# Kernel tuning notes

Measured on AMD Instinct MI355X. Metric: run time of the kernel, lower is better.

## Reference

```python
import jax, jax.numpy as jnp
import numpy as np

# Fixed-step Dormand-Prince RK45 (dopri5) over t in [0, 1].
# torchdiffeq's dopri5 is adaptive; an adaptive while-loop is not
# reverse-differentiable in JAX, so we use the same dopri5 tableau with a
# fixed step count, which reproduces the per-step math exactly.
N_STEPS = 64

# dopri5 Butcher tableau (a-matrix rows; b = 5th-order weights = row a7)
A21 = 1/5
A31, A32 = 3/40, 9/40
A41, A42, A43 = 44/45, -56/15, 32/9
A51, A52, A53, A54 = 19372/6561, -25360/2187, 64448/6561, -212/729
A61, A62, A63, A64, A65 = 9017/3168, -355/33, 46732/5247, 49/176, -5103/18656
B1, B3, B4, B5, B6 = 35/384, 500/1113, 125/192, -2187/6784, 11/84


def setup_inputs() -> dict:
    key = jax.random.key(0)
    ks = jax.random.split(key, 7)
    data_dim, hidden_dim, batch = 512, 1024, 4096
    s1 = 1.0 / np.sqrt(data_dim)
    s2 = 1.0 / np.sqrt(hidden_dim)
    return {
        "x":  jax.random.normal(ks[0], (batch, data_dim), jnp.float32),
        "W1": jax.random.normal(ks[1], (hidden_dim, data_dim), jnp.float32) * s1,
        "b1": jax.random.normal(ks[2], (hidden_dim,), jnp.float32) * s1,
        "W2": jax.random.normal(ks[3], (hidden_dim, hidden_dim), jnp.float32) * s2,
        "b2": jax.random.normal(ks[4], (hidden_dim,), jnp.float32) * s2,
        "W3": jax.random.normal(ks[5], (data_dim, hidden_dim), jnp.float32) * s2,
        "b3": jax.random.normal(ks[6], (data_dim,), jnp.float32) * s2,
    }


def reference(x, W1, b1, W2, b2, W3, b3):
    def f(y):  # ODEFunc MLP: fc1 -> relu -> fc2 -> relu -> fc3 (autonomous)
        h = jax.nn.relu(y @ W1.T + b1)
        h = jax.nn.relu(h @ W2.T + b2)
        return h @ W3.T + b3

    h = jnp.float32(1.0 / N_STEPS)

    def step(y, _):
        k1 = f(y)
        k2 = f(y + h * (A21 * k1))
        k3 = f(y + h * (A31 * k1 + A32 * k2))
        k4 = f(y + h * (A41 * k1 + A42 * k2 + A43 * k3))
        k5 = f(y + h * (A51 * k1 + A52 * k2 + A53 * k3 + A54 * k4))
        k6 = f(y + h * (A61 * k1 + A62 * k2 + A63 * k3 + A64 * k4 + A65 * k5))
        y_next = y + h * (B1 * k1 + B3 * k3 + B4 * k4 + B5 * k5 + B6 * k6)
        return y_next, None

    y_final, _ = jax.lax.scan(step, x, None, length=N_STEPS)
    return y_final
```

## Files before the change

### kernel.cpp

```cpp
#include <hip/hip_runtime.h>
#include <hip/hip_bf16.h>
#include <stdint.h>
#include <stddef.h>

using bf16_t = __hip_bfloat16;
typedef __attribute__((ext_vector_type(8))) short short8;
typedef __attribute__((ext_vector_type(4))) float f32x4;

__device__ __forceinline__ void gload_lds16(void* lds, const void* g) {
  __builtin_amdgcn_global_load_lds(
      (const __attribute__((address_space(1))) unsigned int*)g,
      (__attribute__((address_space(3))) unsigned int*)lds,
      16, 0, 0);
}

template<int MODE>
__global__ __launch_bounds__(256, 4)
void gemm_bt(const bf16_t* __restrict__ A, const bf16_t* __restrict__ B,
             const float* __restrict__ bias,
             bf16_t* __restrict__ obf,
             bf16_t* __restrict__ kout,
             float* __restrict__ yf_out,
             const float* __restrict__ y_in,
             const bf16_t* __restrict__ kp0, const bf16_t* __restrict__ kp1,
             const bf16_t* __restrict__ kp2, const bf16_t* __restrict__ kp3,
             float c0, float c1, float c2, float c3, float ccur,
             int M, int N, int K, int lgx)
{
  __shared__ __align__(16) bf16_t As[2][64 * 64];
  __shared__ __align__(16) bf16_t Bs[2][64 * 64];

  const int t    = threadIdx.x;
  const int lane = t & 63;
  const int wid  = t >> 6;
  const int wm   = wid >> 1;
  const int wn   = wid & 1;

  const int nwg = gridDim.x, bid = blockIdx.x;
  const int swz = (bid & 7) * (nwg >> 3) + (bid >> 3);
  const int gxm = (1 << lgx) - 1;
  const int bx  = swz & gxm;
  const int by  = swz >> lgx;
  const int bn0 = bx * 64, bm0 = by * 64;

  const bf16_t* Ag = A + (size_t)bm0 * K;
  const bf16_t* Bg = B + (size_t)bn0 * K;

  f32x4 acc[2][2] = {};

  auto stage = [&](int b, int kt) {
    const int k0 = kt * 64;
#pragma unroll
    for (int r = 0; r < 2; ++r) {
      int ch  = t + r * 256;
      int row = ch >> 3, s = ch & 7;
      int sl  = s ^ (row & 7);
      gload_lds16(&As[b][ch * 8], Ag + (size_t)row * K + k0 + sl * 8);
    }
#pragma unroll
    for (int r = 0; r < 2; ++r) {
      int ch  = t + r * 256;
      int row = ch >> 3, s = ch & 7;
      int sl  = s ^ (row & 7);
      gload_lds16(&Bs[b][ch * 8], Bg + (size_t)row * K + k0 + sl * 8);
    }
  };

  const int nt = K >> 6;
  stage(0, 0);

  const int ro = lane & 15;
  const int ks = lane >> 4;

  for (int tt = 0; tt < nt; ++tt) {
    const int c = tt & 1;
    asm volatile("s_waitcnt vmcnt(0)" ::: "memory");
    __builtin_amdgcn_s_barrier();
    asm volatile("" ::: "memory");

    if (tt + 1 < nt) stage(c ^ 1, tt + 1);

#pragma unroll
    for (int kk = 0; kk < 2; ++kk) {
      short8 af[2], bfr[2];
      const int slot = kk * 4 + ks;
#pragma unroll
      for (int mi = 0; mi < 2; ++mi) {
        int row = wm * 32 + mi * 16 + ro;
        int ch  = row * 8 + (slot ^ (row & 7));
        af[mi]  = *(const short8*)&As[c][ch * 8];
      }
#pragma unroll
      for (int ni = 0; ni < 2; ++ni) {
        int row = wn * 32 + ni * 16 + ro;
        int ch  = row * 8 + (slot ^ (row & 7));
        bfr[ni] = *(const short8*)&Bs[c][ch * 8];
      }
      __builtin_amdgcn_s_setprio(1);
#pragma unroll
      for (int mi = 0; mi < 2; ++mi)
#pragma unroll
        for (int ni = 0; ni < 2; ++ni)
          acc[mi][ni] = __builtin_amdgcn_mfma_f32_16x16x32_bf16(
              af[mi], bfr[ni], acc[mi][ni], 0, 0, 0);
      __builtin_amdgcn_s_setprio(0);
    }
  }

  const int rb = bm0 + wm * 32;
  const int cb = bn0 + wn * 32;
#pragma unroll
  for (int mi = 0; mi < 2; ++mi) {
#pragma unroll
    for (int ni = 0; ni < 2; ++ni) {
      const int col = cb + ni * 16 + ro;
      const float bv = bias[col];
#pragma unroll
      for (int r = 0; r < 4; ++r) {
        const int row = rb + mi * 16 + (lane >> 4) * 4 + r;
        const size_t idx = (size_t)row * N + col;
        float v = acc[mi][ni][r] + bv;
        if (MODE == 0) {
          obf[idx] = __float2bfloat16(fmaxf(v, 0.f));
        } else {
          if (MODE == 1) kout[idx] = __float2bfloat16(v);
          float z = y_in[idx] + ccur * v;
          if (kp0) z += c0 * __bfloat162float(kp0[idx]);
          if (kp1) z += c1 * __bfloat162float(kp1[idx]);
          if (kp2) z += c2 * __bfloat162float(kp2[idx]);
          if (kp3) z += c3 * __bfloat162float(kp3[idx]);
          if (MODE == 2) yf_out[idx] = z;
          obf[idx] = __float2bfloat16(z);
        }
      }
    }
  }
}

__global__ void init_all(const float* __restrict__ x,
                         const float* __restrict__ W1,
                         const float* __restrict__ W2,
                         const float* __restrict__ W3,
                         bf16_t* __restrict__ W1b, bf16_t* __restrict__ W2b,
                         bf16_t* __restrict__ W3b,
                         float* __restrict__ y, bf16_t* __restrict__ yb,
                         int n1, int n2, int n3, int ny)
{
  const int gt = blockIdx.x * blockDim.x + threadIdx.x;
  const int gs = gridDim.x * blockDim.x;
  auto cvt4 = [&](const float* in, bf16_t* outp, int n) {
    for (int i = gt * 4; i < n; i += gs * 4) {
      float4 v = *(const float4*)(in + i);
      bf16_t o[4] = {__float2bfloat16(v.x), __float2bfloat16(v.y),
                     __float2bfloat16(v.z), __float2bfloat16(v.w)};
      *(uint64_t*)(outp + i) = *(uint64_t*)o;
    }
  };
  cvt4(W1, W1b, n1);
  cvt4(W2, W2b, n2);
  cvt4(W3, W3b, n3);
  for (int i = gt * 4; i < ny; i += gs * 4) {
    float4 v = *(const float4*)(x + i);
    *(float4*)(y + i) = v;
    bf16_t o[4] = {__float2bfloat16(v.x), __float2bfloat16(v.y),
                   __float2bfloat16(v.z), __float2bfloat16(v.w)};
    *(uint64_t*)(yb + i) = *(uint64_t*)o;
  }
}

extern "C" void kernel_launch(void* const* d_in, const int* in_sizes, int n_in,
                              void* d_out, int out_size, void* d_ws, size_t ws_size,
                              hipStream_t stream)
{
  const float* x  = (const float*)d_in[0];
  const float* W1 = (const float*)d_in[1];
  const float* b1 = (const float*)d_in[2];
  const float* W2 = (const float*)d_in[3];
  const float* b2 = (const float*)d_in[4];
  const float* W3 = (const float*)d_in[5];
  const float* b3 = (const float*)d_in[6];

  const int data   = in_sizes[6];
  const int hidden = in_sizes[2];
  const int batch  = in_sizes[0] / data;

  char* ws = (char*)d_ws;
  size_t off = 0;
  auto alloc = [&](size_t bytes) -> void* {
    off = (off + 255) & ~(size_t)255;
    void* p = ws + off;
    off += bytes;
    return p;
  };
  const size_t nyd = (size_t)batch * data;
  const size_t nh  = (size_t)batch * hidden;

  float*  y   = (float*)alloc(nyd * 4);
  bf16_t* yb  = (bf16_t*)alloc(nyd * 2);
  bf16_t* zb  = (bf16_t*)alloc(nyd * 2);
  bf16_t* h1  = (bf16_t*)alloc(nh * 2);
  bf16_t* h2  = (bf16_t*)alloc(nh * 2);
  bf16_t* k1  = (bf16_t*)alloc(nyd * 2);
  bf16_t* k2  = (bf16_t*)alloc(nyd * 2);
  bf16_t* k3  = (bf16_t*)alloc(nyd * 2);
  bf16_t* k4  = (bf16_t*)alloc(nyd * 2);
  bf16_t* k5  = (bf16_t*)alloc(nyd * 2);
  bf16_t* W1b = (bf16_t*)alloc((size_t)hidden * data * 2);
  bf16_t* W2b = (bf16_t*)alloc((size_t)hidden * hidden * 2);
  bf16_t* W3b = (bf16_t*)alloc((size_t)data * hidden * 2);

  init_all<<<2048, 256, 0, stream>>>(x, W1, W2, W3, W1b, W2b, W3b, y, yb,
                                     hidden * data, hidden * hidden,
                                     data * hidden, (int)nyd);

  const double hh = 1.0 / 64.0;
  const float hA21 = (float)(hh * (1.0/5.0));
  const float hA31 = (float)(hh * (3.0/40.0)),    hA32 = (float)(hh * (9.0/40.0));
  const float hA41 = (float)(hh * (44.0/45.0)),   hA42 = (float)(hh * (-56.0/15.0)),
              hA43 = (float)(hh * (32.0/9.0));
  const float hA51 = (float)(hh * (19372.0/6561.0)),  hA52 = (float)(hh * (-25360.0/2187.0)),
              hA53 = (float)(hh * (64448.0/6561.0)),  hA54 = (float)(hh * (-212.0/729.0));
  const float hA61 = (float)(hh * (9017.0/3168.0)),   hA62 = (float)(hh * (-355.0/33.0)),
              hA63 = (float)(hh * (46732.0/5247.0)),  hA64 = (float)(hh * (49.0/176.0)),
              hA65 = (float)(hh * (-5103.0/18656.0));
  const float hB1 = (float)(hh * (35.0/384.0)),   hB3 = (float)(hh * (500.0/1113.0)),
              hB4 = (float)(hh * (125.0/192.0)),  hB5 = (float)(hh * (-2187.0/6784.0)),
              hB6 = (float)(hh * (11.0/84.0));

  const dim3 blk(256);
  const int gridH = (hidden / 64) * (batch / 64);
  const int grid3 = (data / 64) * (batch / 64);
  const int lgxH = 4, lgx3 = 3;

  auto mlp_front = [&](const bf16_t* zin) {
    gemm_bt<0><<<gridH, blk, 0, stream>>>(
        zin, W1b, b1, h1, nullptr, nullptr, nullptr,
        nullptr, nullptr, nullptr, nullptr, 0.f, 0.f, 0.f, 0.f, 0.f,
        batch, hidden, data, lgxH);
    gemm_bt<0><<<gridH, blk, 0, stream>>>(
        h1, W2b, b2, h2, nullptr, nullptr, nullptr,
        nullptr, nullptr, nullptr, nullptr, 0.f, 0.f, 0.f, 0.f, 0.f,
        batch, hidden, hidden, lgxH);
  };

  auto stage_k = [&](bf16_t* kout, const bf16_t* p0, float cc0, const bf16_t* p1, float cc1,
                     const bf16_t* p2, float cc2, const bf16_t* p3, float cc3, float ccur) {
    gemm_bt<1><<<grid3, blk, 0, stream>>>(
        h2, W3b, b3, zb, kout, nullptr, y,
        p0, p1, p2, p3, cc0, cc1, cc2, cc3, ccur,
        batch, data, hidden, lgx3);
  };

  for (int step = 0; step < 64; ++step) {
    mlp_front(yb);
    stage_k(k1, nullptr, 0.f, nullptr, 0.f, nullptr, 0.f, nullptr, 0.f, hA21);
    mlp_front(zb);
    stage_k(k2, k1, hA31, nullptr, 0.f, nullptr, 0.f, nullptr, 0.f, hA32);
    mlp_front(zb);
    stage_k(k3, k1, hA41, k2, hA42, nullptr, 0.f, nullptr, 0.f, hA43);
    mlp_front(zb);
    stage_k(k4, k1, hA51, k2, hA52, k3, hA53, nullptr, 0.f, hA54);
    mlp_front(zb);
    stage_k(k5, k1, hA61, k2, hA62, k3, hA63, k4, hA64, hA65);
    mlp_front(zb);
    float* yf = (step == 63) ? (float*)d_out : y;
    gemm_bt<2><<<grid3, blk, 0, stream>>>(
        h2, W3b, b3, yb, nullptr, yf, y,
        k1, k3, k4, k5, hB1, hB3, hB4, hB5, hB6,
        batch, data, hidden, lgx3);
  }
}
```

Before: 18.22 ms.

## Load B fragments directly to registers and enlarge M tile for hidden GEMMs

The GEMM kernel becomes a templated core. It stages only A through LDS and loads the B (weight) MFMA fragments straight from global memory into registers, double-buffered. The hidden-layer GEMMs use a 128-row M tile (MFRAG=4) with launch bounds lowered to 2 waves per SIMD, which halves their grid and improves A reuse. This removes B LDS traffic and barriers, at the cost of uncoalesced direct global loads of B, more register pressure, and a main loop unrolled by two that assumes an even K-tile count.

```diff
diff --git a/kernel.cpp b/kernel.cpp
--- a/kernel.cpp
+++ b/kernel.cpp
@@ -14,21 +14,21 @@
       16, 0, 0);
 }
 
-template<int MODE>
-__global__ __launch_bounds__(256, 4)
-void gemm_bt(const bf16_t* __restrict__ A, const bf16_t* __restrict__ B,
-             const float* __restrict__ bias,
-             bf16_t* __restrict__ obf,
-             bf16_t* __restrict__ kout,
-             float* __restrict__ yf_out,
-             const float* __restrict__ y_in,
-             const bf16_t* __restrict__ kp0, const bf16_t* __restrict__ kp1,
-             const bf16_t* __restrict__ kp2, const bf16_t* __restrict__ kp3,
-             float c0, float c1, float c2, float c3, float ccur,
-             int M, int N, int K, int lgx)
+template<int MFRAG, int MODE>
+__device__ __forceinline__ void gemm_core(
+    const bf16_t* __restrict__ A, const bf16_t* __restrict__ B,
+    const float* __restrict__ bias,
+    bf16_t* __restrict__ obf,
+    bf16_t* __restrict__ kout,
+    float* __restrict__ yf_out,
+    const float* __restrict__ y_in,
+    const bf16_t* __restrict__ kp0, const bf16_t* __restrict__ kp1,
+    const bf16_t* __restrict__ kp2, const bf16_t* __restrict__ kp3,
+    float c0, float c1, float c2, float c3, float ccur,
+    int M, int N, int K, int lgx)
 {
-  __shared__ __align__(16) bf16_t As[2][64 * 64];
-  __shared__ __align__(16) bf16_t Bs[2][64 * 64];
+  constexpr int BM = 32 * MFRAG;
+  __shared__ __align__(16) bf16_t As[2][BM * 64];
 
   const int t    = threadIdx.x;
   const int lane = t & 63;
@@ -41,76 +41,86 @@
   const int gxm = (1 << lgx) - 1;
   const int bx  = swz & gxm;
   const int by  = swz >> lgx;
-  const int bn0 = bx * 64, bm0 = by * 64;
+  const int bn0 = bx * 64, bm0 = by * BM;
+
+  const int ro = lane & 15;
+  const int ks = lane >> 4;
 
   const bf16_t* Ag = A + (size_t)bm0 * K;
-  const bf16_t* Bg = B + (size_t)bn0 * K;
-
-  f32x4 acc[2][2] = {};
-
-  auto stage = [&](int b, int kt) {
+  const bf16_t* Bcol = B + (size_t)(bn0 + wn * 32 + ro) * K + ks * 8;
+
+  auto stageA = [&](int b, int kt) {
     const int k0 = kt * 64;
 #pragma unroll
-    for (int r = 0; r < 2; ++r) {
+    for (int r = 0; r < MFRAG; ++r) {
       int ch  = t + r * 256;
       int row = ch >> 3, s = ch & 7;
       int sl  = s ^ (row & 7);
       gload_lds16(&As[b][ch * 8], Ag + (size_t)row * K + k0 + sl * 8);
     }
-#pragma unroll
-    for (int r = 0; r < 2; ++r) {
-      int ch  = t + r * 256;
-      int row = ch >> 3, s = ch & 7;
-      int sl  = s ^ (row & 7);
-      gload_lds16(&Bs[b][ch * 8], Bg + (size_t)row * K + k0 + sl * 8);
+  };
+  auto loadB = [&](short8* dst, int kt) {
+#pragma unroll
+    for (int ni = 0; ni < 2; ++ni)
+#pragma unroll
+      for (int kk = 0; kk < 2; ++kk)
+        dst[ni * 2 + kk] =
+            *(const short8*)(Bcol + (size_t)ni * 16 * K + kt * 64 + kk * 32);
+  };
+
+  f32x4 acc[MFRAG][2] = {};
+
+  auto compute = [&](const bf16_t* lds, const short8* bfr) {
+#pragma unroll
+    for (int kk = 0; kk < 2; ++kk) {
+      short8 af[MFRAG];
+      const int slot = kk * 4 + ks;
+#pragma unroll
+      for (int mi = 0; mi < MFRAG; ++mi) {
+        int row = wm * (MFRAG * 16) + mi * 16 + ro;
+        int ch  = row * 8 + (slot ^ (row & 7));
+        af[mi]  = *(const short8*)&lds[ch * 8];
+      }
+      __builtin_amdgcn_s_setprio(1);
+#pragma unroll
+      for (int mi = 0; mi < MFRAG; ++mi)
+#pragma unroll
+        for (int ni = 0; ni < 2; ++ni)
+          acc[mi][ni] = __builtin_amdgcn_mfma_f32_16x16x32_bf16(
+              af[mi], bfr[ni * 2 + kk], acc[mi][ni], 0, 0, 0);
+      __builtin_amdgcn_s_setprio(0);
     }
   };
 
   const int nt = K >> 6;
-  stage(0, 0);
-
-  const int ro = lane & 15;
-  const int ks = lane >> 4;
-
-  for (int tt = 0; tt < nt; ++tt) {
-    const int c = tt & 1;
+  short8 b0[4], b1[4];
+  stageA(0, 0);
+  loadB(b0, 0);
+
+  for (int tt = 0; tt < nt; tt += 2) {
     asm volatile("s_waitcnt vmcnt(0)" ::: "memory");
     __builtin_amdgcn_s_barrier();
     asm volatile("" ::: "memory");
-
-    if (tt + 1 < nt) stage(c ^ 1, tt + 1);
-
-#pragma unroll
-    for (int kk = 0; kk < 2; ++kk) {
-      short8 af[2], bfr[2];
-      const int slot = kk * 4 + ks;
-#pragma unroll
-      for (int mi = 0; mi < 2; ++mi) {
-        int row = wm * 32 + mi * 16 + ro;
-        int ch  = row * 8 + (slot ^ (row & 7));
-        af[mi]  = *(const short8*)&As[c][ch * 8];
-      }
-#pragma unroll
-      for (int ni = 0; ni < 2; ++ni) {
-        int row = wn * 32 + ni * 16 + ro;
-        int ch  = row * 8 + (slot ^ (row & 7));
-        bfr[ni] = *(const short8*)&Bs[c][ch * 8];
-      }
-      __builtin_amdgcn_s_setprio(1);
-#pragma unroll
-      for (int mi = 0; mi < 2; ++mi)
-#pragma unroll
-        for (int ni = 0; ni < 2; ++ni)
-          acc[mi][ni] = __builtin_amdgcn_mfma_f32_16x16x32_bf16(
-              af[mi], bfr[ni], acc[mi][ni], 0, 0, 0);
-      __builtin_amdgcn_s_setprio(0);
-    }
+    {
+      stageA(1, tt + 1);
+      loadB(b1, tt + 1);
+    }
+    compute(As[0], b0);
+
+    asm volatile("s_waitcnt vmcnt(0)" ::: "memory");
+    __builtin_amdgcn_s_barrier();
+    asm volatile("" ::: "memory");
+    if (tt + 2 < nt) {
+      stageA(0, tt + 2);
+      loadB(b0, tt + 2);
+    }
+    compute(As[1], b1);
   }
 
-  const int rb = bm0 + wm * 32;
+  const int rb = bm0 + wm * (MFRAG * 16);
   const int cb = bn0 + wn * 32;
 #pragma unroll
-  for (int mi = 0; mi < 2; ++mi) {
+  for (int mi = 0; mi < MFRAG; ++mi) {
 #pragma unroll
     for (int ni = 0; ni < 2; ++ni) {
       const int col = cb + ni * 16 + ro;
@@ -137,7 +147,25 @@
   }
 }
 
-__global__ void init_all(const float* __restrict__ x,
+#define GEMM_ARGS                                                           \
+    const bf16_t* A, const bf16_t* B, const float* bias, bf16_t* obf,       \
+    bf16_t* kout, float* yf_out, const float* y_in,                         \
+    const bf16_t* kp0, const bf16_t* kp1, const bf16_t* kp2,                \
+    const bf16_t* kp3, float c0, float c1, float c2, float c3, float ccur,  \
+    int M, int N, int K, int lgx
+#define GEMM_PASS A,B,bias,obf,kout,yf_out,y_in,kp0,kp1,kp2,kp3,c0,c1,c2,c3,ccur,M,N,K,lgx
+
+extern "C" __global__ void __launch_bounds__(256, 2) g12relu(GEMM_ARGS) {
+  gemm_core<4, 0>(GEMM_PASS);
+}
+extern "C" __global__ void __launch_bounds__(256, 2) g3kcomb(GEMM_ARGS) {
+  gemm_core<2, 1>(GEMM_PASS);
+}
+extern "C" __global__ void __launch_bounds__(256, 2) g3ycomb(GEMM_ARGS) {
+  gemm_core<2, 2>(GEMM_PASS);
+}
+
+extern "C" __global__ void init_all(const float* __restrict__ x,
                          const float* __restrict__ W1,
                          const float* __restrict__ W2,
                          const float* __restrict__ W3,
@@ -228,16 +256,16 @@
               hB6 = (float)(hh * (11.0/84.0));
 
   const dim3 blk(256);
-  const int gridH = (hidden / 64) * (batch / 64);
+  const int gridH = (hidden / 64) * (batch / 128);
   const int grid3 = (data / 64) * (batch / 64);
   const int lgxH = 4, lgx3 = 3;
 
   auto mlp_front = [&](const bf16_t* zin) {
-    gemm_bt<0><<<gridH, blk, 0, stream>>>(
+    g12relu<<<gridH, blk, 0, stream>>>(
         zin, W1b, b1, h1, nullptr, nullptr, nullptr,
         nullptr, nullptr, nullptr, nullptr, 0.f, 0.f, 0.f, 0.f, 0.f,
         batch, hidden, data, lgxH);
-    gemm_bt<0><<<gridH, blk, 0, stream>>>(
+    g12relu<<<gridH, blk, 0, stream>>>(
         h1, W2b, b2, h2, nullptr, nullptr, nullptr,
         nullptr, nullptr, nullptr, nullptr, 0.f, 0.f, 0.f, 0.f, 0.f,
         batch, hidden, hidden, lgxH);
@@ -245,7 +273,7 @@
 
   auto stage_k = [&](bf16_t* kout, const bf16_t* p0, float cc0, const bf16_t* p1, float cc1,
                      const bf16_t* p2, float cc2, const bf16_t* p3, float cc3, float ccur) {
-    gemm_bt<1><<<grid3, blk, 0, stream>>>(
+    g3kcomb<<<grid3, blk, 0, stream>>>(
         h2, W3b, b3, zb, kout, nullptr, y,
         p0, p1, p2, p3, cc0, cc1, cc2, cc3, ccur,
         batch, data, hidden, lgx3);
@@ -264,7 +292,7 @@
     stage_k(k5, k1, hA61, k2, hA62, k3, hA63, k4, hA64, hA65);
     mlp_front(zb);
     float* yf = (step == 63) ? (float*)d_out : y;
-    gemm_bt<2><<<grid3, blk, 0, stream>>>(
+    g3ycomb<<<grid3, blk, 0, stream>>>(
         h2, W3b, b3, yb, nullptr, yf, y,
         k1, k3, k4, k5, hB1, hB3, hB4, hB5, hB6,
         batch, data, hidden, lgx3);
```

Measured after the change: 24.67 ms. 1.35x slower.

## Fold fc3 into fc1 via precomputed W1·W3 and integrate in hidden space

Applied to the files above, without the earlier changes.

Precomputes W13 = W1·W3 and per-stage folded biases, so each RK stage goes straight from h2 to the next fc1 pre-activation with a 1024x1024 GEMM. Stage pre-activations are kept as bf16 hidden-space vectors. A weighted sum of h2 over the stages is accumulated in the fc2 epilogue, so only one final fc3 GEMM per step updates y. This cuts kernel launches per step and removes the separate fc3-then-fc1 round trip through the 512-wide state. Total FLOPs stay about the same, but the intermediate buffers are twice as wide, and the extra bf16 rounding (W13, stage vectors, the running bf16 sum) adds accuracy risk.

```diff
diff --git a/kernel.cpp b/kernel.cpp
--- a/kernel.cpp
+++ b/kernel.cpp
@@ -15,17 +15,18 @@
 }
 
 template<int MODE>
-__global__ __launch_bounds__(256, 4)
-void gemm_bt(const bf16_t* __restrict__ A, const bf16_t* __restrict__ B,
-             const float* __restrict__ bias,
-             bf16_t* __restrict__ obf,
-             bf16_t* __restrict__ kout,
-             float* __restrict__ yf_out,
-             const float* __restrict__ y_in,
-             const bf16_t* __restrict__ kp0, const bf16_t* __restrict__ kp1,
-             const bf16_t* __restrict__ kp2, const bf16_t* __restrict__ kp3,
-             float c0, float c1, float c2, float c3, float ccur,
-             int M, int N, int K, int lgx)
+__device__ __forceinline__ void gemm_core(
+    const bf16_t* __restrict__ A, const bf16_t* __restrict__ B,
+    const float* __restrict__ bias,
+    bf16_t* __restrict__ obf,
+    bf16_t* __restrict__ aux,
+    bf16_t* __restrict__ vout,
+    float* __restrict__ yf_out,
+    const float* __restrict__ y_in,
+    const bf16_t* __restrict__ p0, const bf16_t* __restrict__ p1,
+    const bf16_t* __restrict__ p2, const bf16_t* __restrict__ p3,
+    float c0, float c1, float c2, float c3, float ccur, int hinit,
+    int M, int N, int K, int lgx)
 {
   __shared__ __align__(16) bf16_t As[2][64 * 64];
   __shared__ __align__(16) bf16_t Bs[2][64 * 64];
@@ -77,7 +78,6 @@
     asm volatile("s_waitcnt vmcnt(0)" ::: "memory");
     __builtin_amdgcn_s_barrier();
     asm volatile("" ::: "memory");
-
     if (tt + 1 < nt) stage(c ^ 1, tt + 1);
 
 #pragma unroll
@@ -114,22 +114,35 @@
 #pragma unroll
     for (int ni = 0; ni < 2; ++ni) {
       const int col = cb + ni * 16 + ro;
-      const float bv = bias[col];
+      const float bv = bias ? bias[col] : 0.f;
 #pragma unroll
       for (int r = 0; r < 4; ++r) {
         const int row = rb + mi * 16 + (lane >> 4) * 4 + r;
         const size_t idx = (size_t)row * N + col;
-        float v = acc[mi][ni][r] + bv;
+        const float a = acc[mi][ni][r];
         if (MODE == 0) {
-          obf[idx] = __float2bfloat16(fmaxf(v, 0.f));
+          float v = fmaxf(a + bv, 0.f);
+          obf[idx] = __float2bfloat16(v);
+          if (aux) {
+            float hs = ccur * v + (hinit ? 0.f : __bfloat162float(aux[idx]));
+            aux[idx] = __float2bfloat16(hs);
+          }
+        } else if (MODE == 1) {
+          vout[idx] = __float2bfloat16(a);
+          float u = __bfloat162float(aux[idx]) + ccur * a + bv;
+          if (p0) u += c0 * __bfloat162float(p0[idx]);
+          if (p1) u += c1 * __bfloat162float(p1[idx]);
+          if (p2) u += c2 * __bfloat162float(p2[idx]);
+          if (p3) u += c3 * __bfloat162float(p3[idx]);
+          obf[idx] = __float2bfloat16(fmaxf(u, 0.f));
+        } else if (MODE == 2) {
+          aux[idx] = __float2bfloat16(a);
+          obf[idx] = __float2bfloat16(fmaxf(a + bv, 0.f));
+        } else if (MODE == 3) {
+          obf[idx] = __float2bfloat16(a);
         } else {
-          if (MODE == 1) kout[idx] = __float2bfloat16(v);
-          float z = y_in[idx] + ccur * v;
-          if (kp0) z += c0 * __bfloat162float(kp0[idx]);
-          if (kp1) z += c1 * __bfloat162float(kp1[idx]);
-          if (kp2) z += c2 * __bfloat162float(kp2[idx]);
-          if (kp3) z += c3 * __bfloat162float(kp3[idx]);
-          if (MODE == 2) yf_out[idx] = z;
+          float z = y_in[idx] + a + ccur * bv;
+          yf_out[idx] = z;
           obf[idx] = __float2bfloat16(z);
         }
       }
@@ -137,14 +150,31 @@
   }
 }
 
-__global__ void init_all(const float* __restrict__ x,
-                         const float* __restrict__ W1,
-                         const float* __restrict__ W2,
-                         const float* __restrict__ W3,
-                         bf16_t* __restrict__ W1b, bf16_t* __restrict__ W2b,
-                         bf16_t* __restrict__ W3b,
-                         float* __restrict__ y, bf16_t* __restrict__ yb,
-                         int n1, int n2, int n3, int ny)
+#define GARGS                                                               \
+    const bf16_t* A, const bf16_t* B, const float* bias, bf16_t* obf,       \
+    bf16_t* aux, bf16_t* vout, float* yf_out, const float* y_in,            \
+    const bf16_t* p0, const bf16_t* p1, const bf16_t* p2, const bf16_t* p3, \
+    float c0, float c1, float c2, float c3, float ccur, int hinit,          \
+    int M, int N, int K, int lgx
+#define GPASS A,B,bias,obf,aux,vout,yf_out,y_in,p0,p1,p2,p3,c0,c1,c2,c3,ccur,hinit,M,N,K,lgx
+
+extern "C" __global__ void __launch_bounds__(256, 4) gmid(GARGS) { gemm_core<0>(GPASS); }
+extern "C" __global__ void __launch_bounds__(256, 4) gvst(GARGS) { gemm_core<1>(GPASS); }
+extern "C" __global__ void __launch_bounds__(256, 4) gyw1(GARGS) { gemm_core<2>(GPASS); }
+extern "C" __global__ void __launch_bounds__(256, 4) gw13(GARGS) { gemm_core<3>(GPASS); }
+extern "C" __global__ void __launch_bounds__(256, 4) gyup(GARGS) { gemm_core<4>(GPASS); }
+
+extern "C" __global__ void init_all(
+    const float* __restrict__ x,
+    const float* __restrict__ W1, const float* __restrict__ W2,
+    const float* __restrict__ W3,
+    const float* __restrict__ b1, const float* __restrict__ b3,
+    bf16_t* __restrict__ W1b, bf16_t* __restrict__ W2b,
+    bf16_t* __restrict__ W3b, bf16_t* __restrict__ W3Tb,
+    float* __restrict__ y, bf16_t* __restrict__ yb,
+    float* __restrict__ bS2, float* __restrict__ bS3, float* __restrict__ bS4,
+    float* __restrict__ bS5, float* __restrict__ bS6,
+    float s2, float s3, float s4, float s5, float s6)
 {
   const int gt = blockIdx.x * blockDim.x + threadIdx.x;
   const int gs = gridDim.x * blockDim.x;
@@ -156,15 +186,30 @@
       *(uint64_t*)(outp + i) = *(uint64_t*)o;
     }
   };
-  cvt4(W1, W1b, n1);
-  cvt4(W2, W2b, n2);
-  cvt4(W3, W3b, n3);
-  for (int i = gt * 4; i < ny; i += gs * 4) {
+  cvt4(W1, W1b, 1024 * 512);
+  cvt4(W2, W2b, 1024 * 1024);
+  cvt4(W3, W3b, 512 * 1024);
+  for (int i = gt; i < 512 * 1024; i += gs) {
+    int d = i >> 10, j = i & 1023;
+    W3Tb[(size_t)j * 512 + d] = __float2bfloat16(W3[i]);
+  }
+  for (int i = gt * 4; i < 4096 * 512; i += gs * 4) {
     float4 v = *(const float4*)(x + i);
     *(float4*)(y + i) = v;
     bf16_t o[4] = {__float2bfloat16(v.x), __float2bfloat16(v.y),
                    __float2bfloat16(v.z), __float2bfloat16(v.w)};
     *(uint64_t*)(yb + i) = *(uint64_t*)o;
+  }
+  if (gt < 1024) {
+    float c13 = 0.f;
+    const float* wr = W1 + (size_t)gt * 512;
+    for (int d = 0; d < 512; ++d) c13 += b3[d] * wr[d];
+    const float bb = b1[gt];
+    bS2[gt] = bb + s2 * c13;
+    bS3[gt] = bb + s3 * c13;
+    bS4[gt] = bb + s4 * c13;
+    bS5[gt] = bb + s5 * c13;
+    bS6[gt] = bb + s6 * c13;
   }
 }
 
@@ -180,9 +225,7 @@
   const float* W3 = (const float*)d_in[5];
   const float* b3 = (const float*)d_in[6];
 
-  const int data   = in_sizes[6];
-  const int hidden = in_sizes[2];
-  const int batch  = in_sizes[0] / data;
+  constexpr int BATCH = 4096, DATA = 512, HID = 1024;
 
   char* ws = (char*)d_ws;
   size_t off = 0;
@@ -192,26 +235,30 @@
     off += bytes;
     return p;
   };
-  const size_t nyd = (size_t)batch * data;
-  const size_t nh  = (size_t)batch * hidden;
-
-  float*  y   = (float*)alloc(nyd * 4);
-  bf16_t* yb  = (bf16_t*)alloc(nyd * 2);
-  bf16_t* zb  = (bf16_t*)alloc(nyd * 2);
-  bf16_t* h1  = (bf16_t*)alloc(nh * 2);
-  bf16_t* h2  = (bf16_t*)alloc(nh * 2);
-  bf16_t* k1  = (bf16_t*)alloc(nyd * 2);
-  bf16_t* k2  = (bf16_t*)alloc(nyd * 2);
-  bf16_t* k3  = (bf16_t*)alloc(nyd * 2);
-  bf16_t* k4  = (bf16_t*)alloc(nyd * 2);
-  bf16_t* k5  = (bf16_t*)alloc(nyd * 2);
-  bf16_t* W1b = (bf16_t*)alloc((size_t)hidden * data * 2);
-  bf16_t* W2b = (bf16_t*)alloc((size_t)hidden * hidden * 2);
-  bf16_t* W3b = (bf16_t*)alloc((size_t)data * hidden * 2);
-
-  init_all<<<2048, 256, 0, stream>>>(x, W1, W2, W3, W1b, W2b, W3b, y, yb,
-                                     hidden * data, hidden * hidden,
-                                     data * hidden, (int)nyd);
+  const size_t nyd = (size_t)BATCH * DATA;
+  const size_t nh  = (size_t)BATCH * HID;
+
+  float*  y    = (float*)alloc(nyd * 4);
+  bf16_t* yb   = (bf16_t*)alloc(nyd * 2);
+  bf16_t* h1b  = (bf16_t*)alloc(nh * 2);
+  bf16_t* h2b  = (bf16_t*)alloc(nh * 2);
+  bf16_t* yw1b = (bf16_t*)alloc(nh * 2);
+  bf16_t* hsumb= (bf16_t*)alloc(nh * 2);
+  bf16_t* v1   = (bf16_t*)alloc(nh * 2);
+  bf16_t* v2   = (bf16_t*)alloc(nh * 2);
+  bf16_t* v3   = (bf16_t*)alloc(nh * 2);
+  bf16_t* v4   = (bf16_t*)alloc(nh * 2);
+  bf16_t* v5   = (bf16_t*)alloc(nh * 2);
+  bf16_t* W1b  = (bf16_t*)alloc((size_t)HID * DATA * 2);
+  bf16_t* W2b  = (bf16_t*)alloc((size_t)HID * HID * 2);
+  bf16_t* W3b  = (bf16_t*)alloc((size_t)DATA * HID * 2);
+  bf16_t* W3Tb = (bf16_t*)alloc((size_t)HID * DATA * 2);
+  bf16_t* W13b = (bf16_t*)alloc((size_t)HID * HID * 2);
+  float*  bS2  = (float*)alloc(HID * 4);
+  float*  bS3  = (float*)alloc(HID * 4);
+  float*  bS4  = (float*)alloc(HID * 4);
+  float*  bS5  = (float*)alloc(HID * 4);
+  float*  bS6  = (float*)alloc(HID * 4);
 
   const double hh = 1.0 / 64.0;
   const float hA21 = (float)(hh * (1.0/5.0));
@@ -226,47 +273,59 @@
   const float hB1 = (float)(hh * (35.0/384.0)),   hB3 = (float)(hh * (500.0/1113.0)),
               hB4 = (float)(hh * (125.0/192.0)),  hB5 = (float)(hh * (-2187.0/6784.0)),
               hB6 = (float)(hh * (11.0/84.0));
+  const float s2 = hA21, s3 = hA31 + hA32, s4 = hA41 + hA42 + hA43,
+              s5 = hA51 + hA52 + hA53 + hA54,
+              s6 = hA61 + hA62 + hA63 + hA64 + hA65;
+
+  init_all<<<2048, 256, 0, stream>>>(x, W1, W2, W3, b1, b3,
+                                     W1b, W2b, W3b, W3Tb, y, yb,
+                                     bS2, bS3, bS4, bS5, bS6,
+                                     s2, s3, s4, s5, s6);
 
   const dim3 blk(256);
-  const int gridH = (hidden / 64) * (batch / 64);
-  const int grid3 = (data / 64) * (batch / 64);
-  const int lgxH = 4, lgx3 = 3;
-
-  auto mlp_front = [&](const bf16_t* zin) {
-    gemm_bt<0><<<gridH, blk, 0, stream>>>(
-        zin, W1b, b1, h1, nullptr, nullptr, nullptr,
-        nullptr, nullptr, nullptr, nullptr, 0.f, 0.f, 0.f, 0.f, 0.f,
-        batch, hidden, data, lgxH);
-    gemm_bt<0><<<gridH, blk, 0, stream>>>(
-        h1, W2b, b2, h2, nullptr, nullptr, nullptr,
-        nullptr, nullptr, nullptr, nullptr, 0.f, 0.f, 0.f, 0.f, 0.f,
-        batch, hidden, hidden, lgxH);
-  };
-
-  auto stage_k = [&](bf16_t* kout, const bf16_t* p0, float cc0, const bf16_t* p1, float cc1,
-                     const bf16_t* p2, float cc2, const bf16_t* p3, float cc3, float ccur) {
-    gemm_bt<1><<<grid3, blk, 0, stream>>>(
-        h2, W3b, b3, zb, kout, nullptr, y,
-        p0, p1, p2, p3, cc0, cc1, cc2, cc3, ccur,
-        batch, data, hidden, lgx3);
+  const int gridN = (HID / 64) * (BATCH / 64);
+  const int gridY = (DATA / 64) * (BATCH / 64);
+  const int gridW = (HID / 64) * (HID / 64);
+
+  gw13<<<gridW, blk, 0, stream>>>(
+      W1b, W3Tb, nullptr, W13b, nullptr, nullptr, nullptr, nullptr,
+      nullptr, nullptr, nullptr, nullptr, 0.f, 0.f, 0.f, 0.f, 0.f, 0,
+      HID, HID, DATA, 4);
+
+  auto G2 = [&](bf16_t* hs, float coef, int hinit) {
+    gmid<<<gridN, blk, 0, stream>>>(
+        h1b, W2b, b2, h2b, hs, nullptr, nullptr, nullptr,
+        nullptr, nullptr, nullptr, nullptr,
+        0.f, 0.f, 0.f, 0.f, coef, hinit, BATCH, HID, HID, 4);
+  };
+  auto V = [&](bf16_t* vo, const float* bS, float ccur,
+               const bf16_t* q0, float cc0, const bf16_t* q1, float cc1,
+               const bf16_t* q2, float cc2, const bf16_t* q3, float cc3) {
+    gvst<<<gridN, blk, 0, stream>>>(
+        h2b, W13b, bS, h1b, yw1b, vo, nullptr, nullptr,
+        q0, q1, q2, q3, cc0, cc1, cc2, cc3, ccur, 0, BATCH, HID, HID, 4);
   };
 
   for (int step = 0; step < 64; ++step) {
-    mlp_front(yb);
-    stage_k(k1, nullptr, 0.f, nullptr, 0.f, nullptr, 0.f, nullptr, 0.f, hA21);
-    mlp_front(zb);
-    stage_k(k2, k1, hA31, nullptr, 0.f, nullptr, 0.f, nullptr, 0.f, hA32);
-    mlp_front(zb);
-    stage_k(k3, k1, hA41, k2, hA42, nullptr, 0.f, nullptr, 0.f, hA43);
-    mlp_front(zb);
-    stage_k(k4, k1, hA51, k2, hA52, k3, hA53, nullptr, 0.f, hA54);
-    mlp_front(zb);
-    stage_k(k5, k1, hA61, k2, hA62, k3, hA63, k4, hA64, hA65);
-    mlp_front(zb);
+    gyw1<<<gridN, blk, 0, stream>>>(
+        yb, W1b, b1, h1b, yw1b, nullptr, nullptr, nullptr,
+        nullptr, nullptr, nullptr, nullptr,
+        0.f, 0.f, 0.f, 0.f, 0.f, 0, BATCH, HID, DATA, 4);
+    G2(hsumb, hB1, 1);
+    V(v1, bS2, hA21, nullptr,0,nullptr,0,nullptr,0,nullptr,0);
+    G2(nullptr, 0.f, 0);
+    V(v2, bS3, hA32, v1,hA31, nullptr,0,nullptr,0,nullptr,0);
+    G2(hsumb, hB3, 0);
+    V(v3, bS4, hA43, v1,hA41, v2,hA42, nullptr,0,nullptr,0);
+    G2(hsumb, hB4, 0);
+    V(v4, bS5, hA54, v1,hA51, v2,hA52, v3,hA53, nullptr,0);
+    G2(hsumb, hB5, 0);
+    V(v5, bS6, hA65, v1,hA61, v2,hA62, v3,hA63, v4,hA64);
+    G2(hsumb, hB6, 0);
     float* yf = (step == 63) ? (float*)d_out : y;
-    gemm_bt<2><<<grid3, blk, 0, stream>>>(
-        h2, W3b, b3, yb, nullptr, yf, y,
-        k1, k3, k4, k5, hB1, hB3, hB4, hB5, hB6,
-        batch, data, hidden, lgx3);
+    gyup<<<gridY, blk, 0, stream>>>(
+        hsumb, W3b, b3, yb, nullptr, nullptr, yf, y,
+        nullptr, nullptr, nullptr, nullptr,
+        0.f, 0.f, 0.f, 0.f, (float)hh, 0, BATCH, DATA, HID, 3);
   }
 }
```

New measurement: 17.50 ms. 4.0% less time.
